# Kernel tuning notes

Hardware: AMD Instinct MI355X
Metric: run time of the kernel (lower is better)

## Reference

```python
import jax, jax.numpy as jnp
import numpy as np
import math

T = 2048; HID = 2048; H = 16; KV = 8; G = H // KV; D = 128
GH = 128; BS = 64; NB = T // BS
EPS = 1e-6; RATIO = 0.2; SCALE = 1.0 / math.sqrt(D)


def _rope_tables(length, dim, theta=1000000.0):
    inv = 1.0 / (theta ** (np.arange(0, dim, 2, dtype=np.float32) / dim))
    f = np.outer(np.arange(length, dtype=np.float32), inv)
    emb = np.concatenate([f, f], axis=-1)
    return jnp.asarray(np.cos(emb)), jnp.asarray(np.sin(emb))


def _rot_half(x):
    d = x.shape[-1] // 2
    return jnp.concatenate([-x[..., d:], x[..., :d]], axis=-1)


def _apply_rope(x, cos, sin):
    # x: [T, nH, D], cos/sin: [T, D] broadcast over head dim
    return x * cos[:, None, :] + _rot_half(x) * sin[:, None, :]


def _rmsnorm(x, w, eps=EPS):
    xf = x.astype(jnp.float32)
    v = jnp.mean(xf * xf, axis=-1, keepdims=True)
    return (w * (xf * jax.lax.rsqrt(v + eps))).astype(x.dtype)


def setup_inputs() -> dict:
    key = jax.random.key(0)
    ks = jax.random.split(key, 8)
    s = 0.02
    hidden_states = jax.random.normal(ks[0], (T, HID), jnp.float32)
    Wq = jax.random.normal(ks[1], (HID, H * D), jnp.float32) * s
    Wk = jax.random.normal(ks[2], (HID, KV * D), jnp.float32) * s
    Wv = jax.random.normal(ks[3], (HID, KV * D), jnp.float32) * s
    Wo = jax.random.normal(ks[4], (H * D, HID), jnp.float32) * s
    q_norm_w = jnp.ones((D,), jnp.float32)
    k_norm_w = jnp.ones((D,), jnp.float32)
    gate_wq = jax.random.normal(ks[5], (D, GH), jnp.float32) * s
    gate_wk = jax.random.normal(ks[6], (D, GH), jnp.float32) * s
    cos, sin = _rope_tables(T, D)
    cos_gq, sin_gq = _rope_tables(T, GH)
    cos_blk, sin_blk = _rope_tables(NB, GH)
    # causal block mask: query t may attend to key block j iff j <= t // BS
    block_attention_mask = (jnp.arange(T)[:, None] // BS) >= jnp.arange(NB)[None, :]
    return dict(hidden_states=hidden_states, Wq=Wq, Wk=Wk, Wv=Wv, Wo=Wo,
                q_norm_w=q_norm_w, k_norm_w=k_norm_w, gate_wq=gate_wq, gate_wk=gate_wk,
                cos=cos, sin=sin, cos_gq=cos_gq, sin_gq=sin_gq,
                cos_blk=cos_blk, sin_blk=sin_blk,
                block_attention_mask=block_attention_mask)


def reference(hidden_states, Wq, Wk, Wv, Wo, q_norm_w, k_norm_w, gate_wq, gate_wk,
              cos, sin, cos_gq, sin_gq, cos_blk, sin_blk, block_attention_mask):
    q = (hidden_states @ Wq).reshape(T, H, D)
    k = (hidden_states @ Wk).reshape(T, KV, D)
    v = (hidden_states @ Wv).reshape(T, KV, D)
    q = _rmsnorm(q, q_norm_w)
    k = _rmsnorm(k, k_norm_w)

    # ---- gate network on un-roped q/k: q-head avg-pool to KV heads, k avg-pool per block ----
    q_pool = q.reshape(T, KV, G, D).mean(axis=2)            # [T, KV, D]
    gq = _apply_rope(q_pool @ gate_wq, cos_gq, sin_gq)      # [T, KV, GH]
    k_blk = k.reshape(NB, BS, KV, D).mean(axis=1)           # [NB, KV, D]
    gk = _apply_rope(k_blk @ gate_wk, cos_blk, sin_blk)     # [NB, KV, GH]
    gate_scores = jnp.einsum('tkg,nkg->ktn', gq, gk) / math.sqrt(GH)  # [KV, T, NB]
    predict_mask = jnp.where(block_attention_mask[None], gate_scores, -1e9)

    # ---- main attention (RoPE + GQA causal softmax attention) ----
    qr = _apply_rope(q, cos, sin)
    kr = _apply_rope(k, cos, sin)
    kr_rep = jnp.repeat(kr, G, axis=1)                      # [T, H, D]
    v_rep = jnp.repeat(v, G, axis=1)
    logits = jnp.einsum('thd,shd->hts', qr, kr_rep) * SCALE  # [H, T, T]
    causal = jnp.tril(jnp.ones((T, T), bool))
    logits = jnp.where(causal[None], logits, -jnp.inf)
    probs = jax.nn.softmax(logits, axis=-1)
    attn_output = jnp.einsum('hts,shd->thd', probs, v_rep).reshape(T, H * D) @ Wo

    # ---- pooled ground-truth block mask: attention mass per key block ----
    pooled = probs.reshape(H, T, NB, BS).sum(axis=-1)        # [H, T, NB]
    gt = pooled.reshape(KV, G, T, NB).max(axis=1)            # max_pool3d over head groups -> [KV,T,NB]
    gt = jnp.where(block_attention_mask[None], gt, 0.0)
    gt = gt / (gt.sum(axis=-1, keepdims=True) + 1e-9)

    # ---- KLDiv gate loss on the tail slice (bsz = 1) ----
    start = int(T * RATIO)
    tgt = gt[:, start:, :]                                   # [KV, L, NB]
    logp = jax.nn.log_softmax(predict_mask[:, start:, :], axis=-1)
    safe_t = jnp.where(tgt > 0, tgt, 1.0)
    kl = jnp.where(tgt > 0, tgt * (jnp.log(safe_t) - logp), 0.0)
    gate_loss = kl.reshape(KV, -1).mean(axis=-1).sum()       # KLDivLoss(reduction='mean') per kv head, summed, /bsz(=1)
    return attn_output, gate_loss
```

## Files before the change

### kernel.cpp

```cpp
#include <hip/hip_runtime.h>

#define T_ 2048
#define HID_ 2048
#define H_ 16
#define KV_ 8
#define G_ 2
#define D_ 128
#define GH_ 128
#define BS_ 64
#define NB_ 32
#define START_ 409
#define TG0_ 384
#define SCALE_ 0.08838834764831845f
#define MFIX_ 8.0f
#define HT_ 32768

typedef __attribute__((ext_vector_type(8))) short short8_t;
typedef __attribute__((ext_vector_type(4))) float float4_t;
typedef __attribute__((ext_vector_type(8))) unsigned short ushort8_t;
typedef __attribute__((ext_vector_type(4))) unsigned short ushort4_t;

__device__ __forceinline__ float wave_sum(float v) {
#pragma unroll
  for (int o = 32; o > 0; o >>= 1) v += __shfl_xor(v, o, 64);
  return v;
}
__device__ __forceinline__ unsigned short f2bf(float x) {
  unsigned int u = __float_as_uint(x);
  unsigned int r = (u + 0x7fffu + ((u >> 16) & 1u)) >> 16;
  return (unsigned short)r;
}
__device__ __forceinline__ float bf2f(unsigned short h) {
  return __uint_as_float(((unsigned int)h) << 16);
}

__device__ __forceinline__ void gload16(const void* g, void* l) {
  __builtin_amdgcn_global_load_lds((const __attribute__((address_space(1))) unsigned int*)g,
                                   (__attribute__((address_space(3))) unsigned int*)l, 16, 0, 0);
}

__device__ __forceinline__ void castT_dev(const float* __restrict__ in,
                                          unsigned short* __restrict__ out, int K, int N,
                                          int ldin, int bx, int by,
                                          unsigned short (*tile)[72], int tid) {
  int k0 = by * 64, n0 = bx * 64;
  int tx = tid & 63, ty4 = tid >> 6;
#pragma unroll
  for (int i = 0; i < 16; ++i) {
    int ky = ty4 * 16 + i;
    tile[tx][ky] = f2bf(in[(size_t)(k0 + ky) * ldin + n0 + tx]);
  }
  __syncthreads();
#pragma unroll
  for (int i = 0; i < 16; ++i) {
    int ny = ty4 * 16 + i;
    out[(size_t)(n0 + ny) * K + k0 + tx] = tile[ny][tx];
  }
}

__global__ __launch_bounds__(256) void castT(const float* __restrict__ in,
                                             unsigned short* __restrict__ out,
                                             int K, int N, int ldin) {
  __shared__ unsigned short tile[64][72];
  castT_dev(in, out, K, N, ldin, blockIdx.x, blockIdx.y, tile, threadIdx.x);
}

__global__ __launch_bounds__(256) void prep_cast(const float* __restrict__ hs,
                                                 const float* __restrict__ Wq,
                                                 const float* __restrict__ Wk,
                                                 const float* __restrict__ Wv,
                                                 const float* __restrict__ Wo,
                                                 const float* __restrict__ gwq,
                                                 const float* __restrict__ gwk,
                                                 unsigned short* __restrict__ hsb,
                                                 unsigned short* __restrict__ WqkvT,
                                                 unsigned short* __restrict__ WoT,
                                                 unsigned short* __restrict__ gwqT,
                                                 unsigned short* __restrict__ gwkT) {
  __shared__ unsigned short tile[64][72];
  int id = blockIdx.x, tid = threadIdx.x;
  if (id < 4096) {
    int i = id * 256 + tid;
    float4 v = ((const float4*)hs)[i];
    ushort4_t o = {f2bf(v.x), f2bf(v.y), f2bf(v.z), f2bf(v.w)};
    *(ushort4_t*)(hsb + (size_t)i * 4) = o;
  } else if (id < 5120) {
    int t = id - 4096;
    castT_dev(Wq, WqkvT, 2048, 2048, 2048, t & 31, t >> 5, tile, tid);
  } else if (id < 5632) {
    int t = id - 5120;
    castT_dev(Wk, WqkvT + (size_t)2048 * 2048, 2048, 1024, 1024, t & 15, t >> 4, tile, tid);
  } else if (id < 6144) {
    int t = id - 5632;
    castT_dev(Wv, WqkvT + (size_t)3072 * 2048, 2048, 1024, 1024, t & 15, t >> 4, tile, tid);
  } else if (id < 7168) {
    int t = id - 6144;
    castT_dev(Wo, WoT, 2048, 2048, 2048, t & 31, t >> 5, tile, tid);
  } else if (id < 7172) {
    int t = id - 7168;
    castT_dev(gwq, gwqT, 128, 128, 128, t & 1, t >> 1, tile, tid);
  } else {
    int t = id - 7172;
    castT_dev(gwk, gwkT, 128, 128, 128, t & 1, t >> 1, tile, tid);
  }
}

__global__ __launch_bounds__(256) void gemm_bf16_v3(const unsigned short* __restrict__ A,
                                                    const unsigned short* __restrict__ Bt,
                                                    float* __restrict__ C,
                                                    int M, int N, int K, int ldc) {
  __shared__ unsigned short As[128 * 64];
  __shared__ unsigned short Bs[128 * 64];
  int tid = threadIdx.x;
  int wid = tid >> 6, lane = tid & 63;
  int quad = lane >> 4, l16 = lane & 15;
  int wm = wid & 1, wn = wid >> 1;
  int m0 = blockIdx.y * 128, n0 = blockIdx.x * 128;
  const unsigned short* gA[4];
  const unsigned short* gB[4];
#pragma unroll
  for (int it = 0; it < 4; ++it) {
    int line = wid * 32 + it * 8 + (lane >> 3);
    int chunk = (lane & 7) ^ (line & 7);
    gA[it] = A + (size_t)(m0 + line) * K + chunk * 8;
    gB[it] = Bt + (size_t)(n0 + line) * K + chunk * 8;
  }
  float4_t acc[4][4];
#pragma unroll
  for (int i = 0; i < 4; ++i)
#pragma unroll
    for (int j = 0; j < 4; ++j) acc[i][j] = (float4_t){0.f, 0.f, 0.f, 0.f};
  for (int k0 = 0; k0 < K; k0 += 64) {
    __syncthreads();
#pragma unroll
    for (int it = 0; it < 4; ++it) {
      gload16(gA[it] + k0, As + (wid * 32 + it * 8) * 64);
      gload16(gB[it] + k0, Bs + (wid * 32 + it * 8) * 64);
    }
    __syncthreads();
    short8_t a[2][4], b[2][4];
#pragma unroll
    for (int ks = 0; ks < 2; ++ks) {
      int sw = ((ks * 4 + quad) ^ (l16 & 7)) * 8;
#pragma unroll
      for (int i = 0; i < 4; ++i) {
        a[ks][i] = *(const short8_t*)&As[(wm * 64 + i * 16 + l16) * 64 + sw];
        b[ks][i] = *(const short8_t*)&Bs[(wn * 64 + i * 16 + l16) * 64 + sw];
      }
    }
#pragma unroll
    for (int ks = 0; ks < 2; ++ks)
#pragma unroll
      for (int i = 0; i < 4; ++i)
#pragma unroll
        for (int j = 0; j < 4; ++j)
          acc[i][j] = __builtin_amdgcn_mfma_f32_16x16x32_bf16(a[ks][i], b[ks][j], acc[i][j], 0, 0, 0);
  }
#pragma unroll
  for (int i = 0; i < 4; ++i)
#pragma unroll
    for (int j = 0; j < 4; ++j)
#pragma unroll
      for (int reg = 0; reg < 4; ++reg)
        C[(size_t)(m0 + wm * 64 + i * 16 + quad * 4 + reg) * ldc + n0 + wn * 64 + j * 16 + l16] =
            acc[i][j][reg];
}

__global__ __launch_bounds__(128) void norm_rope_fused(const float* __restrict__ qkvf,
                                                       const float* __restrict__ qw,
                                                       const float* __restrict__ kw,
                                                       const float* __restrict__ cosT,
                                                       const float* __restrict__ sinT,
                                                       unsigned short* __restrict__ qbf,
                                                       unsigned short* __restrict__ qpool_bf,
                                                       unsigned short* __restrict__ kbf,
                                                       float* __restrict__ knorm) {
  int t = blockIdx.x, d = threadIdx.x;
  if (blockIdx.y < 8) {
    int kv = blockIdx.y;
    size_t i0 = (size_t)t * 4096 + (kv * G_) * D_ + d;
    float x0 = qkvf[i0], x1 = qkvf[i0 + D_];
    __shared__ float sred[2][2];
    float s0 = wave_sum(x0 * x0), s1 = wave_sum(x1 * x1);
    if ((d & 63) == 0) { sred[0][d >> 6] = s0; sred[1][d >> 6] = s1; }
    __syncthreads();
    float wv = qw[d];
    float n0 = x0 * rsqrtf((sred[0][0] + sred[0][1]) * (1.f / D_) + 1e-6f) * wv;
    float n1 = x1 * rsqrtf((sred[1][0] + sred[1][1]) * (1.f / D_) + 1e-6f) * wv;
    if (t >= TG0_) qpool_bf[((size_t)(t - TG0_) * KV_ + kv) * D_ + d] = f2bf(0.5f * (n0 + n1));
    __shared__ float sh[2][D_];
    sh[0][d] = n0; sh[1][d] = n1;
    __syncthreads();
    float c = cosT[t * D_ + d], s = sinT[t * D_ + d];
    float r0 = (d < 64) ? -sh[0][d + 64] : sh[0][d - 64];
    float r1 = (d < 64) ? -sh[1][d + 64] : sh[1][d - 64];
    qbf[((size_t)(t * H_) + kv * G_) * D_ + d] = f2bf(n0 * c + r0 * s);
    qbf[((size_t)(t * H_) + kv * G_ + 1) * D_ + d] = f2bf(n1 * c + r1 * s);
  } else {
    int kv = blockIdx.y - 8;
    float x = qkvf[(size_t)t * 4096 + 2048 + kv * D_ + d];
    __shared__ float sredk[2];
    float s0 = wave_sum(x * x);
    if ((d & 63) == 0) sredk[d >> 6] = s0;
    __syncthreads();
    float nk = x * rsqrtf((sredk[0] + sredk[1]) * (1.f / D_) + 1e-6f) * kw[d];
    knorm[(size_t)(t * KV_ + kv) * D_ + d] = nk;
    __shared__ float shk[D_];
    shk[d] = nk;
    __syncthreads();
    float rot = (d < 64) ? -shk[d + 64] : shk[d - 64];
    kbf[(size_t)(t * KV_ + kv) * D_ + d] = f2bf(nk * cosT[t * D_ + d] + rot * sinT[t * D_ + d]);
  }
}

__global__ __launch_bounds__(128) void kblk_kernel(const float* __restrict__ knorm,
                                                   unsigned short* __restrict__ kblk_bf) {
  int n = blockIdx.x, kv = blockIdx.y, d = threadIdx.x;
  float s = 0.f;
  for (int i = 0; i < BS_; ++i) s += knorm[((size_t)(n * BS_ + i) * KV_ + kv) * D_ + d];
  kblk_bf[(size_t)(n * KV_ + kv) * D_ + d] = f2bf(s * (1.f / BS_));
}

__global__ __launch_bounds__(128) void rope_g_fused(float* __restrict__ gq, float* __restrict__ gk,
                                                    const float* __restrict__ cosG,
                                                    const float* __restrict__ sinG,
                                                    const float* __restrict__ cosB,
                                                    const float* __restrict__ sinB) {
  int r = blockIdx.x, kvh = blockIdx.y, d = threadIdx.x;
  float* x;
  size_t base;
  float c_, s_;
  if (r < NB_) {
    x = gk;
    base = (size_t)(r * KV_ + kvh) * GH_;
    c_ = cosB[r * GH_ + d]; s_ = sinB[r * GH_ + d];
  } else {
    int rr = r - NB_;
    x = gq;
    base = (size_t)(rr * KV_ + kvh) * GH_;
    c_ = cosG[(size_t)(TG0_ + rr) * GH_ + d]; s_ = sinG[(size_t)(TG0_ + rr) * GH_ + d];
  }
  __shared__ float sh[GH_];
  sh[d] = x[base + d];
  __syncthreads();
  float rot = (d < 64) ? -sh[d + 64] : sh[d - 64];
  x[base + d] = sh[d] * c_ + rot * s_;
}

__global__ __launch_bounds__(128, 2) void attn_mfma(const unsigned short* __restrict__ qbf,
                                                    const unsigned short* __restrict__ kbf,
                                                    const unsigned short* __restrict__ vt,
                                                    unsigned short* __restrict__ opart,
                                                    float* __restrict__ lpart,
                                                    float* __restrict__ pooledraw) {
  int h = blockIdx.x;
  int y = blockIdx.y;
  int tile, p;
  {
    int qd = y >> 4, r = y & 15;
    if (qd == 0)      { tile = r;       p = 0; }
    else if (qd == 1) { tile = 16 + r;  p = 0; }
    else if (qd == 2) { tile = 15 - r;  p = 1; }
    else              { tile = 31 - r;  p = 1; }
  }
  int t0 = tile * 64;
  int tid = threadIdx.x;
  int wid = tid >> 6, lane = tid & 63;
  int quad = lane >> 4, l16 = lane & 15;
  int kv = h >> 1;
  __shared__ unsigned short Ks[64 * 128];
  __shared__ unsigned short Vs[128 * 64];
  __shared__ unsigned short Ps[2][32 * 64];

  const unsigned short* kbase[8];
  const unsigned short* vbase[8];
#pragma unroll
  for (int it = 0; it < 8; ++it) {
    int seg = wid * 8 + it;
    int krow = seg * 4 + (lane >> 4);
    int kchk = lane & 15;
    kbase[it] = kbf + ((size_t)krow * KV_ + kv) * D_ + ((kchk ^ (krow & 7)) << 3);
    int vrow = seg * 8 + (lane >> 3);
    int vchk = lane & 7;
    vbase[it] = vt + (size_t)(kv * 128 + vrow) * T_ + ((vchk ^ (vrow & 7)) << 3);
  }

  short8_t qf[2][4];
#pragma unroll
  for (int rs = 0; rs < 2; ++rs) {
    int tq = t0 + wid * 32 + rs * 16 + l16;
#pragma unroll
    for (int kb = 0; kb < 4; ++kb)
      qf[rs][kb] = *(const short8_t*)&qbf[((size_t)tq * H_ + h) * D_ + kb * 32 + quad * 8];
  }

  const short one_bf = (short)0x3F80;
  short8_t ones = {one_bf, one_bf, one_bf, one_bf, one_bf, one_bf, one_bf, one_bf};

  float l_[2][4] = {};
  float pacc[2][2][4] = {};
  float4_t o[2][8];
#pragma unroll
  for (int rs = 0; rs < 2; ++rs)
#pragma unroll
    for (int j = 0; j < 8; ++j) o[rs][j] = (float4_t){0.f, 0.f, 0.f, 0.f};

  for (int c = p; c <= tile; c += 2) {
    __syncthreads();
#pragma unroll
    for (int it = 0; it < 8; ++it) {
      gload16(kbase[it] + (size_t)c * 65536, Ks + (wid * 8 + it) * 512);
      gload16(vbase[it] + c * 64, Vs + (wid * 8 + it) * 512);
    }
    __syncthreads();

    float4_t s[4][2];
#pragma unroll
    for (int j = 0; j < 4; ++j) {
      short8_t kf[4];
#pragma unroll
      for (int kb = 0; kb < 4; ++kb)
        kf[kb] = *(const short8_t*)&Ks[(j * 16 + l16) * 128 + (((kb * 4 + quad) ^ (l16 & 7)) << 3)];
#pragma unroll
      for (int rs = 0; rs < 2; ++rs) {
        float4_t a = (float4_t){0.f, 0.f, 0.f, 0.f};
#pragma unroll
        for (int kb = 0; kb < 4; ++kb)
          a = __builtin_amdgcn_mfma_f32_16x16x32_bf16(qf[rs][kb], kf[kb], a, 0, 0, 0);
        s[j][rs] = a;
      }
    }
    if (c == tile) {
#pragma unroll
      for (int rs = 0; rs < 2; ++rs)
#pragma unroll
        for (int reg = 0; reg < 4; ++reg) {
          int trow = t0 + wid * 32 + rs * 16 + quad * 4 + reg;
#pragma unroll
          for (int j = 0; j < 4; ++j) {
            float pv = __expf(s[j][rs][reg] * SCALE_ - MFIX_);
            s[j][rs][reg] = (c * 64 + j * 16 + l16 <= trow) ? pv : 0.f;
          }
        }
    } else {
#pragma unroll
      for (int j = 0; j < 4; ++j)
#pragma unroll
        for (int rs = 0; rs < 2; ++rs)
#pragma unroll
          for (int reg = 0; reg < 4; ++reg)
            s[j][rs][reg] = __expf(s[j][rs][reg] * SCALE_ - MFIX_);
    }
#pragma unroll
    for (int j = 0; j < 4; ++j)
#pragma unroll
      for (int rs = 0; rs < 2; ++rs)
#pragma unroll
        for (int reg = 0; reg < 4; ++reg) {
          int rr = rs * 16 + quad * 4 + reg;
          Ps[wid][rr * 64 + ((((j * 2) + (l16 >> 3)) ^ (rr & 7)) << 3) + (l16 & 7)] =
              f2bf(s[j][rs][reg]);
        }
    float4_t pool[2];
    pool[0] = (float4_t){0.f, 0.f, 0.f, 0.f};
    pool[1] = (float4_t){0.f, 0.f, 0.f, 0.f};
#pragma unroll
    for (int ks = 0; ks < 2; ++ks) {
      short8_t pf[2];
#pragma unroll
      for (int rs = 0; rs < 2; ++rs) {
        int rr = rs * 16 + l16;
        pf[rs] = *(const short8_t*)&Ps[wid][rr * 64 + (((ks * 4 + quad) ^ (rr & 7)) << 3)];
        pool[rs] = __builtin_amdgcn_mfma_f32_16x16x32_bf16(pf[rs], ones, pool[rs], 0, 0, 0);
      }
#pragma unroll
      for (int jt = 0; jt < 8; ++jt) {
        short8_t vf = *(const short8_t*)&Vs[(jt * 16 + l16) * 64 + (((ks * 4 + quad) ^ (l16 & 7)) << 3)];
#pragma unroll
        for (int rs = 0; rs < 2; ++rs)
          o[rs][jt] = __builtin_amdgcn_mfma_f32_16x16x32_bf16(pf[rs], vf, o[rs][jt], 0, 0, 0);
      }
    }
    int half16 = (c >> 4) & 1, cl = c & 15;
#pragma unroll
    for (int rs = 0; rs < 2; ++rs)
#pragma unroll
      for (int reg = 0; reg < 4; ++reg) {
        l_[rs][reg] += pool[rs][reg];
        if (l16 == cl) pacc[half16][rs][reg] = pool[rs][reg];
      }
  }
  unsigned short* op = opart + (size_t)p * (T_ * H_ * D_);
#pragma unroll
  for (int rs = 0; rs < 2; ++rs)
#pragma unroll
    for (int jt = 0; jt < 8; ++jt)
#pragma unroll
      for (int reg = 0; reg < 4; ++reg) {
        int trow = t0 + wid * 32 + rs * 16 + quad * 4 + reg;
        op[(size_t)trow * (H_ * D_) + h * D_ + jt * 16 + l16] = f2bf(o[rs][jt][reg]);
      }
  if (l16 == 0) {
#pragma unroll
    for (int rs = 0; rs < 2; ++rs)
#pragma unroll
      for (int reg = 0; reg < 4; ++reg) {
        int trow = t0 + wid * 32 + rs * 16 + quad * 4 + reg;
        lpart[p * HT_ + h * T_ + trow] = l_[rs][reg];
      }
  }
  if ((l16 & 1) == p) {
#pragma unroll
    for (int rs = 0; rs < 2; ++rs)
#pragma unroll
      for (int reg = 0; reg < 4; ++reg) {
        int trow = t0 + wid * 32 + rs * 16 + quad * 4 + reg;
        pooledraw[((size_t)h * T_ + trow) * NB_ + l16] = pacc[0][rs][reg];
        pooledraw[((size_t)h * T_ + trow) * NB_ + 16 + l16] = pacc[1][rs][reg];
      }
  }
}

__global__ __launch_bounds__(256) void merge_o(const unsigned short* __restrict__ opart,
                                               const float* __restrict__ lpart,
                                               unsigned short* __restrict__ attnb) {
  int i = (blockIdx.x * 256 + threadIdx.x) * 4;
  int t = i >> 11, h = (i & 2047) >> 7;
  float inv = 1.f / (lpart[h * T_ + t] + lpart[HT_ + h * T_ + t]);
  ushort4_t a = *(const ushort4_t*)(opart + i);
  ushort4_t b = *(const ushort4_t*)(opart + (size_t)(T_ * H_ * D_) + i);
  ushort4_t r;
#pragma unroll
  for (int k = 0; k < 4; ++k) r[k] = f2bf((bf2f(a[k]) + bf2f(b[k])) * inv);
  *(ushort4_t*)(attnb + i) = r;
}

__global__ __launch_bounds__(256) void gate_loss2(const float* __restrict__ gq,
                                                  const float* __restrict__ gk,
                                                  const float* __restrict__ pooledraw,
                                                  const float* __restrict__ lpart,
                                                  float* __restrict__ klsum) {
  int kv = blockIdx.x;
  int sub = threadIdx.x >> 5;
  int n = threadIdx.x & 31;
  int tloc = blockIdx.y * 8 + sub;
  bool act = tloc < (T_ - START_);
  int t = START_ + (act ? tloc : 0);
  const float4* a = (const float4*)(gq + ((size_t)(t - TG0_) * KV_ + kv) * GH_);
  const float4* b = (const float4*)(gk + (size_t)(n * KV_ + kv) * GH_);
  float dot = 0.f;
#pragma unroll
  for (int d4 = 0; d4 < 32; ++d4) {
    float4 av = a[d4], bv = b[d4];
    dot += av.x * bv.x + av.y * bv.y + av.z * bv.z + av.w * bv.w;
  }
  bool valid = (t / BS_) >= n;
  float score = valid ? dot * SCALE_ : -1e9f;
  float M = score;
#pragma unroll
  for (int o = 16; o > 0; o >>= 1) M = fmaxf(M, __shfl_xor(M, o, 64));
  float e = __expf(score - M);
  float Z = e;
#pragma unroll
  for (int o = 16; o > 0; o >>= 1) Z += __shfl_xor(Z, o, 64);
  float logZ = M + logf(Z);
  float g = 0.f;
  if (valid) {
    int h0 = kv * G_, h1 = h0 + 1;
    float inv0 = 1.f / (lpart[h0 * T_ + t] + lpart[HT_ + h0 * T_ + t]);
    float inv1 = 1.f / (lpart[h1 * T_ + t] + lpart[HT_ + h1 * T_ + t]);
    float p0 = pooledraw[((size_t)h0 * T_ + t) * NB_ + n] * inv0;
    float p1 = pooledraw[((size_t)h1 * T_ + t) * NB_ + n] * inv1;
    g = fmaxf(p0, p1);
  }
  float gs = g;
#pragma unroll
  for (int o = 16; o > 0; o >>= 1) gs += __shfl_xor(gs, o, 64);
  float tgt = g / (gs + 1e-9f);
  float kl = (tgt > 0.f) ? tgt * (logf(tgt) - (score - logZ)) : 0.f;
  float ks = kl;
#pragma unroll
  for (int o = 16; o > 0; o >>= 1) ks += __shfl_xor(ks, o, 64);
  if (n == 0 && act) klsum[kv * (T_ - START_) + tloc] = ks;
}

__global__ __launch_bounds__(256) void finalize_loss(const float* __restrict__ klsum,
                                                     float* __restrict__ out) {
  const int n = KV_ * (T_ - START_);
  float s = 0.f;
  for (int i = threadIdx.x; i < n; i += 256) s += klsum[i];
  s = wave_sum(s);
  __shared__ float sh[4];
  if ((threadIdx.x & 63) == 0) sh[threadIdx.x >> 6] = s;
  __syncthreads();
  if (threadIdx.x == 0)
    out[0] = (sh[0] + sh[1] + sh[2] + sh[3]) * (1.f / ((float)(T_ - START_) * NB_));
}

extern "C" void kernel_launch(void* const* d_in, const int* in_sizes, int n_in,
                              void* d_out, int out_size, void* d_ws, size_t ws_size,
                              hipStream_t stream) {
  const float* hs   = (const float*)d_in[0];
  const float* Wq   = (const float*)d_in[1];
  const float* Wk   = (const float*)d_in[2];
  const float* Wv   = (const float*)d_in[3];
  const float* Wo   = (const float*)d_in[4];
  const float* qw   = (const float*)d_in[5];
  const float* kw   = (const float*)d_in[6];
  const float* gwq  = (const float*)d_in[7];
  const float* gwk  = (const float*)d_in[8];
  const float* cosT = (const float*)d_in[9];
  const float* sinT = (const float*)d_in[10];
  const float* cosG = (const float*)d_in[11];
  const float* sinG = (const float*)d_in[12];
  const float* cosB = (const float*)d_in[13];
  const float* sinB = (const float*)d_in[14];
  float* out = (float*)d_out;
  float* ws = (float*)d_ws;
  const size_t MEG = 1048576;

  float*          qkvf      = ws;
  unsigned short* opart     = (unsigned short*)ws;
  unsigned short* attnb     = (unsigned short*)(ws + 4 * MEG);
  float*          pooledraw = ws + 6 * MEG;
  float*          lpart     = ws + 7 * MEG;
  float*          klsum     = ws + 7 * MEG + 65536;
  unsigned short* WqkvT     = (unsigned short*)(ws + 8 * MEG);
  unsigned short* qbf       = WqkvT;
  unsigned short* kbf       = WqkvT + 4 * MEG;
  unsigned short* vt        = WqkvT + 6 * MEG;
  unsigned short* hsb       = (unsigned short*)(ws + 12 * MEG);
  float*          knorm     = ws + 12 * MEG;
  unsigned short* WoT       = (unsigned short*)(ws + 14 * MEG);
  unsigned short* qpool_bf  = (unsigned short*)(ws + 16 * MEG);
  float*          gq        = ws + 17 * MEG;
  unsigned short* kblk_bf   = (unsigned short*)(ws + 18 * MEG + 786432);
  float*          gk        = ws + 18 * MEG + 819200;
  unsigned short* gwqT      = (unsigned short*)(ws + 18 * MEG + 851968);
  unsigned short* gwkT      = (unsigned short*)(ws + 18 * MEG + 860160);

  prep_cast<<<7176, 256, 0, stream>>>(hs, Wq, Wk, Wv, Wo, gwq, gwk, hsb, WqkvT, WoT, gwqT, gwkT);
  gemm_bf16_v3<<<dim3(32, 16), 256, 0, stream>>>(hsb, WqkvT, qkvf, 2048, 4096, 2048, 4096);
  norm_rope_fused<<<dim3(T_, 16), 128, 0, stream>>>(qkvf, qw, kw, cosT, sinT, qbf, qpool_bf,
                                                    kbf, knorm);
  castT<<<dim3(16, 32), 256, 0, stream>>>(qkvf + 3072, vt, T_, 1024, 4096);
  kblk_kernel<<<dim3(NB_, KV_), 128, 0, stream>>>(knorm, kblk_bf);
  gemm_bf16_v3<<<dim3(1, 104), 256, 0, stream>>>(qpool_bf, gwqT, gq, 13312, 128, 128, 128);
  gemm_bf16_v3<<<dim3(1, 2), 256, 0, stream>>>(kblk_bf, gwkT, gk, 256, 128, 128, 128);
  rope_g_fused<<<dim3(NB_ + (T_ - TG0_), KV_), 128, 0, stream>>>(gq, gk, cosG, sinG, cosB, sinB);
  attn_mfma<<<dim3(H_, 64), 128, 0, stream>>>(qbf, kbf, vt, opart, lpart, pooledraw);
  merge_o<<<4096, 256, 0, stream>>>(opart, lpart, attnb);
  gemm_bf16_v3<<<dim3(16, 16), 256, 0, stream>>>(attnb, WoT, out, 2048, 2048, 2048, 2048);
  gate_loss2<<<dim3(KV_, 205), 256, 0, stream>>>(gq, gk, pooledraw, lpart, klsum);
  finalize_loss<<<1, 256, 0, stream>>>(klsum, out + (size_t)T_ * HID_);
}
```

Before: 367.4 us.

## Load K/V fragments directly from global into registers, drop LDS staging

The attention kernel stops staging K and V tiles in shared memory with block-wide barriers. Each wave now loads its MFMA K and V fragments straight from global memory into registers. The block-to-tile mapping also changes to interleave the two parity halves and order tiles from largest to smallest. This removes the two __syncthreads per iteration and the LDS traffic. In exchange, each of the two waves fetches the same K/V data separately, which doubles global/L2 reads, and register pressure rises under launch_bounds(128,2).

Result: slower. 426.7 us (+16.1%).

```diff
diff --git a/kernel.cpp b/kernel.cpp
--- a/kernel.cpp
+++ b/kernel.cpp
@@ -255,35 +255,14 @@
                                                     float* __restrict__ pooledraw) {
   int h = blockIdx.x;
   int y = blockIdx.y;
-  int tile, p;
-  {
-    int qd = y >> 4, r = y & 15;
-    if (qd == 0)      { tile = r;       p = 0; }
-    else if (qd == 1) { tile = 16 + r;  p = 0; }
-    else if (qd == 2) { tile = 15 - r;  p = 1; }
-    else              { tile = 31 - r;  p = 1; }
-  }
+  int z = y >> 1, p = y & 1;
+  int tile = (z < 16) ? (31 - z) : (z - 16);
   int t0 = tile * 64;
   int tid = threadIdx.x;
   int wid = tid >> 6, lane = tid & 63;
   int quad = lane >> 4, l16 = lane & 15;
   int kv = h >> 1;
-  __shared__ unsigned short Ks[64 * 128];
-  __shared__ unsigned short Vs[128 * 64];
   __shared__ unsigned short Ps[2][32 * 64];
-
-  const unsigned short* kbase[8];
-  const unsigned short* vbase[8];
-#pragma unroll
-  for (int it = 0; it < 8; ++it) {
-    int seg = wid * 8 + it;
-    int krow = seg * 4 + (lane >> 4);
-    int kchk = lane & 15;
-    kbase[it] = kbf + ((size_t)krow * KV_ + kv) * D_ + ((kchk ^ (krow & 7)) << 3);
-    int vrow = seg * 8 + (lane >> 3);
-    int vchk = lane & 7;
-    vbase[it] = vt + (size_t)(kv * 128 + vrow) * T_ + ((vchk ^ (vrow & 7)) << 3);
-  }
 
   short8_t qf[2][4];
 #pragma unroll
@@ -293,6 +272,9 @@
     for (int kb = 0; kb < 4; ++kb)
       qf[rs][kb] = *(const short8_t*)&qbf[((size_t)tq * H_ + h) * D_ + kb * 32 + quad * 8];
   }
+
+  const unsigned short* kL = kbf + ((size_t)l16 * KV_ + kv) * D_ + quad * 8;
+  const unsigned short* vL = vt + ((size_t)(kv * 128 + l16)) * T_ + quad * 8;
 
   const short one_bf = (short)0x3F80;
   short8_t ones = {one_bf, one_bf, one_bf, one_bf, one_bf, one_bf, one_bf, one_bf};
@@ -306,30 +288,31 @@
     for (int j = 0; j < 8; ++j) o[rs][j] = (float4_t){0.f, 0.f, 0.f, 0.f};
 
   for (int c = p; c <= tile; c += 2) {
-    __syncthreads();
-#pragma unroll
-    for (int it = 0; it < 8; ++it) {
-      gload16(kbase[it] + (size_t)c * 65536, Ks + (wid * 8 + it) * 512);
-      gload16(vbase[it] + c * 64, Vs + (wid * 8 + it) * 512);
-    }
-    __syncthreads();
-
+    const unsigned short* kc = kL + (size_t)c * 64 * (KV_ * D_);
+    const unsigned short* vc = vL + c * 64;
+    short8_t kf[4][4];
+#pragma unroll
+    for (int j = 0; j < 4; ++j)
+#pragma unroll
+      for (int kb = 0; kb < 4; ++kb)
+        kf[j][kb] = *(const short8_t*)(kc + (size_t)j * 16 * (KV_ * D_) + kb * 32);
     float4_t s[4][2];
 #pragma unroll
-    for (int j = 0; j < 4; ++j) {
-      short8_t kf[4];
-#pragma unroll
-      for (int kb = 0; kb < 4; ++kb)
-        kf[kb] = *(const short8_t*)&Ks[(j * 16 + l16) * 128 + (((kb * 4 + quad) ^ (l16 & 7)) << 3)];
+    for (int j = 0; j < 4; ++j)
 #pragma unroll
       for (int rs = 0; rs < 2; ++rs) {
         float4_t a = (float4_t){0.f, 0.f, 0.f, 0.f};
 #pragma unroll
         for (int kb = 0; kb < 4; ++kb)
-          a = __builtin_amdgcn_mfma_f32_16x16x32_bf16(qf[rs][kb], kf[kb], a, 0, 0, 0);
+          a = __builtin_amdgcn_mfma_f32_16x16x32_bf16(qf[rs][kb], kf[j][kb], a, 0, 0, 0);
         s[j][rs] = a;
       }
-    }
+    short8_t vf[2][8];
+#pragma unroll
+    for (int ks = 0; ks < 2; ++ks)
+#pragma unroll
+      for (int jt = 0; jt < 8; ++jt)
+        vf[ks][jt] = *(const short8_t*)(vc + (size_t)jt * 16 * T_ + ks * 32);
     if (c == tile) {
 #pragma unroll
       for (int rs = 0; rs < 2; ++rs)
@@ -374,12 +357,10 @@
         pool[rs] = __builtin_amdgcn_mfma_f32_16x16x32_bf16(pf[rs], ones, pool[rs], 0, 0, 0);
       }
 #pragma unroll
-      for (int jt = 0; jt < 8; ++jt) {
-        short8_t vf = *(const short8_t*)&Vs[(jt * 16 + l16) * 64 + (((ks * 4 + quad) ^ (l16 & 7)) << 3)];
+      for (int jt = 0; jt < 8; ++jt)
 #pragma unroll
         for (int rs = 0; rs < 2; ++rs)
-          o[rs][jt] = __builtin_amdgcn_mfma_f32_16x16x32_bf16(pf[rs], vf, o[rs][jt], 0, 0, 0);
-      }
+          o[rs][jt] = __builtin_amdgcn_mfma_f32_16x16x32_bf16(pf[rs], vf[ks][jt], o[rs][jt], 0, 0, 0);
     }
     int half16 = (c >> 4) & 1, cl = c & 15;
 #pragma unroll
```
